# Kernel optimization log

Measured on AMD Instinct MI355X. Metric: run time of the kernel, lower is better.

Reference implementation:

```python
import jax, jax.numpy as jnp
import numpy as np

B, N, F_DIM, G_DIM, E_CAT, N_HEAD = 8, 1024, 128, 64, 2, 4
N_EDGES = 16384
L0 = 256          # NodeEmbedding hidden layer (layers=[256,128] -> last replaced by feature_size)
ALPHA = 0.5       # cfg.alpha
EPS = 1e-5        # BatchNorm eps
SLOPE = 0.01      # leaky_relu default negative slope


def _glorot(k, shape):
    stdv = float(np.sqrt(6.0 / (shape[-2] + shape[-1])))
    return jax.random.uniform(k, shape, jnp.float32, -stdv, stdv)


def setup_inputs() -> dict:
    key = jax.random.key(0)
    ks = jax.random.split(key, 8)
    X = jax.random.normal(ks[0], (B, N, F_DIM), dtype=jnp.float32)
    A = jax.random.randint(ks[1], (B, E_CAT, 2, N_EDGES), 0, N, dtype=jnp.int32)
    Ws = _glorot(ks[2], (E_CAT, N_HEAD * F_DIM, G_DIM))
    Wq = _glorot(ks[3], (E_CAT, N_HEAD * F_DIM, 1))
    Wv = _glorot(ks[4], (E_CAT, N_HEAD * F_DIM, 1))
    W_emb1 = _glorot(ks[5], (F_DIM, N_HEAD * E_CAT * G_DIM))   # Embedding1, bias=False
    W_lin0 = _glorot(ks[6], (L0, F_DIM))                        # NodeEmbedding linear0
    W_lin1 = _glorot(ks[7], (F_DIM, L0))                        # NodeEmbedding linear1
    return {"A": A, "X": X, "Ws": Ws, "Wq": Wq, "Wv": Wv,
            "W_emb1": W_emb1, "W_lin0": W_lin0, "W_lin1": W_lin1, "mini_batch": 1}


def _bn(x):
    # BatchNorm1d in training mode, affine = identity (weight=1, bias=0)
    mu = jnp.mean(x, axis=0)
    var = jnp.var(x, axis=0)  # biased variance, as torch uses for normalization
    return (x - mu) * jax.lax.rsqrt(var + EPS)


def _build_adj(A):
    # torch.sparse_coo_tensor(...).to_dense() sums duplicate edges
    adj = jnp.zeros((B, E_CAT, N, N), jnp.float32)
    b_idx = jnp.arange(B)[:, None, None]
    e_idx = jnp.arange(E_CAT)[None, :, None]
    return adj.at[b_idx, e_idx, A[:, :, 0], A[:, :, 1]].add(1.0)


def reference(A, X, Ws, Wq, Wv, W_emb1, W_lin0, W_lin1, mini_batch):
    Ws_r = Ws.reshape(E_CAT, N_HEAD, F_DIM, G_DIM)
    Wq_r = Wq.reshape(E_CAT, N_HEAD, F_DIM)   # last dim of Wq param is 1
    Wv_r = Wv.reshape(E_CAT, N_HEAD, F_DIM)

    Wh = jnp.einsum('bnf,ehfg->behng', X, Ws_r)   # [B,E,H,N,G]
    q = jnp.einsum('bnf,ehf->behn', X, Wq_r)      # [B,E,H,N]
    v = jnp.einsum('bnf,ehf->behn', X, Wv_r)

    adj = _build_adj(A)                            # [B,E,N,N]
    # e = (Wq @ Wv.T) * E, then leaky_relu and row softmax (dim=1 on [N,N] = last axis)
    scores = q[:, :, :, :, None] * v[:, :, :, None, :] * adj[:, :, None]
    scores = jnp.where(scores >= 0, scores, SLOPE * scores)
    a = jax.nn.softmax(scores, axis=-1)
    H = jnp.einsum('behnm,behmg->behng', a, Wh)    # [B,E,H,N,G]

    # concat over heads: [B,N, head-major (E*G)]
    H = H.transpose(0, 3, 2, 1, 4).reshape(B * N, N_HEAD * E_CAT * G_DIM)
    H = jax.nn.relu(H @ W_emb1.T)
    Xf = X.reshape(B * N, F_DIM)
    H = _bn((1.0 - ALPHA) * H + ALPHA * Xf)

    # NodeEmbedding: Linear -> BN -> ELU -> Linear
    Z = jax.nn.elu(_bn(H @ W_lin0.T))
    Z = Z @ W_lin1.T
    Z = _bn(H + Z)
    return Z.reshape(B, N, F_DIM)
```

## Files before the change

### kernel.cpp

```cpp
#include <hip/hip_runtime.h>
#include <hip/hip_bf16.h>

#define B_    8
#define N_    1024
#define F_    128
#define G_    64
#define EC    2
#define NHD   4
#define NE    16384
#define L0_   256
#define ALPHA_ 0.5f
#define EPS_   1e-5f
#define SLOPE_ 0.01f
#define ROWS  (B_*N_)
#define C1    (NHD*EC*G_)

typedef __attribute__((ext_vector_type(8))) short s8bf;
typedef __attribute__((ext_vector_type(4))) float f32x4;

__device__ __forceinline__ float ldv(const float* p, size_t i) { return p[i]; }
__device__ __forceinline__ float ldv(const __hip_bfloat16* p, size_t i) {
  unsigned short u = *(const unsigned short*)&p[i];
  return __uint_as_float((unsigned)u << 16);
}
__device__ __forceinline__ unsigned short f2b(float f) {
  unsigned u = __float_as_uint(f);
  u = (u + 0x7FFFu + ((u >> 16) & 1u)) >> 16;
  return (unsigned short)u;
}
__device__ __forceinline__ float b2f(unsigned short u) {
  return __uint_as_float((unsigned)u << 16);
}

__device__ __forceinline__ float wmaxf(float v) {
#pragma unroll
  for (int o = 32; o; o >>= 1) v = fmaxf(v, __shfl_xor(v, o, 64));
  return v;
}
__device__ __forceinline__ float wsumf(float v) {
#pragma unroll
  for (int o = 32; o; o >>= 1) v += __shfl_xor(v, o, 64);
  return v;
}

__global__ void k_prep(const unsigned short* Xu, int* flag,
                       const int* A, int* fill, int* colbuf) {
  int bid = blockIdx.x, tid = threadIdx.x;
  if (bid < 512) {
    int idx = bid * 256 + tid;
    unsigned short u = Xu[idx];
    if ((u & 0x7F80u) == 0x7F80u) atomicOr(flag, 1);
  } else {
    int idx = (bid - 512) * 256 + tid;
    int be = idx >> 14, i = idx & (NE - 1);
    int row = A[(size_t)(be * 2) * NE + i];
    int col = A[(size_t)(be * 2 + 1) * NE + i];
    int p = atomicAdd(&fill[be * N_ + row], 1);
    if (p < 64) colbuf[((size_t)(be * N_ + row)) * 64 + p] = col;
  }
}

__device__ __forceinline__ unsigned short cvt_at(const void* p, size_t i, int isf) {
  return isf ? f2b(((const float*)p)[i]) : ((const unsigned short*)p)[i];
}
template <typename T>
__device__ __forceinline__ void proj_qv16(const T* X, const T* Wq, const T* Wv,
                                          float* q, float* v, int pb) {
  int tid = threadIdx.x, lane = tid & 63, w = tid >> 6;
  int sub = lane >> 4, fl = lane & 15;
  int r = pb * 16 + w * 4 + sub;
  int n = r & (N_ - 1); int beh = r >> 10; int be = beh >> 2, h = beh & 3;
  int b = be >> 1, e = be & 1;
  const T* xr = X + (size_t)(b * N_ + n) * F_ + fl * 8;
  const T* wq = Wq + (e * NHD + h) * F_ + fl * 8;
  const T* wv = Wv + (e * NHD + h) * F_ + fl * 8;
  float dq = 0.f, dv = 0.f;
#pragma unroll
  for (int j = 0; j < 8; ++j) {
    float x = ldv(xr, j);
    dq += x * ldv(wq, j); dv += x * ldv(wv, j);
  }
#pragma unroll
  for (int o = 1; o < 16; o <<= 1) {
    dq += __shfl_xor(dq, o, 64); dv += __shfl_xor(dv, o, 64);
  }
  if (fl == 0) { q[r] = dq; v[r] = dv; }
}
__global__ void k_cvt2(const void* X, const void* Ws, const void* We1, const void* Wl1,
                       const void* Wl0, const void* Wq, const void* Wv,
                       unsigned short* Wsb, unsigned short* We1b,
                       unsigned short* Wl1b, unsigned short* Wl0b,
                       float* q, float* v, const int* flag) {
  int isf = *flag;
  int bid = blockIdx.x, t = threadIdx.x;
  if (bid < 256) {
    int i = bid * 256 + t; We1b[i] = cvt_at(We1, i, isf);
  } else if (bid < 384) {
    int i = (bid - 256) * 256 + t; Wl1b[i] = cvt_at(Wl1, i, isf);
  } else if (bid < 512) {
    int i = (bid - 384) * 256 + t; Wl0b[i] = cvt_at(Wl0, i, isf);
  } else if (bid < 768) {
    int i = (bid - 512) * 256 + t;
    int eh = i >> 13, rem = i & 8191;
    int g = rem >> 7, f = rem & 127;
    Wsb[eh * 8192 + g * 128 + f] = cvt_at(Ws, (size_t)eh * 8192 + f * 64 + g, isf);
  } else {
    int pb = bid - 768;
    if (isf) proj_qv16<float>((const float*)X, (const float*)Wq, (const float*)Wv, q, v, pb);
    else     proj_qv16<__hip_bfloat16>((const __hip_bfloat16*)X, (const __hip_bfloat16*)Wq,
                                       (const __hip_bfloat16*)Wv, q, v, pb);
  }
}

template <int K, int NC, int MODE, typename TA>
__device__ __forceinline__ void mfma_core_u(const TA* __restrict__ Araw,
                                            const float* sum, const float* ssq,
                                            const unsigned short* __restrict__ Wb,
                                            int r0, int c0, f32x4* acc) {
  int lane = threadIdx.x & 63; int q = lane >> 4, c15 = lane & 15;
  constexpr int RS = K / 8;
  const s8bf* bp = (const s8bf*)Wb + (size_t)(c0 + c15) * RS + q;
#pragma unroll
  for (int ks = 0; ks < K / 32; ++ks) {
    s8bf a;
    if constexpr (sizeof(TA) == 2) {
      const s8bf* ap = (const s8bf*)Araw + (size_t)(r0 + c15) * RS + q;
      a = ap[ks * 4];
    } else {
      const float* ap = (const float*)Araw + (size_t)(r0 + c15) * K + q * 8 + ks * 32;
      float av[8];
      *(float4*)&av[0] = *(const float4*)ap;
      *(float4*)&av[4] = *(const float4*)(ap + 4);
#pragma unroll
      for (int j = 0; j < 8; ++j) {
        float y = av[j];
        if (MODE) {
          int c = q * 8 + ks * 32 + j;
          float mean = sum[c] * (1.f / ROWS);
          float var = ssq[c] * (1.f / ROWS) - mean * mean;
          y = (y - mean) * rsqrtf(var + EPS_);
          if (MODE == 2) y = (y > 0.f) ? y : (expf(y) - 1.f);
        }
        a[j] = (short)f2b(y);
      }
    }
#pragma unroll
    for (int nc = 0; nc < NC; ++nc) {
      s8bf b = bp[(size_t)nc * 16 * RS + ks * 4];
      acc[nc] = __builtin_amdgcn_mfma_f32_16x16x32_bf16(a, b, acc[nc], 0, 0, 0);
    }
  }
}

__global__ __launch_bounds__(256) void k_whm(const void* X, const unsigned short* Wsb,
                                             unsigned short* Whb, float* S,
                                             const int* flag) {
  int w = threadIdx.x >> 6;
  int r0 = (blockIdx.x * 4 + w) * 16; int eh = blockIdx.y;
  f32x4 acc[4] = {{0,0,0,0},{0,0,0,0},{0,0,0,0},{0,0,0,0}};
  if (*flag)
    mfma_core_u<128, 4, 0, float>((const float*)X, nullptr, nullptr,
                                  Wsb + eh * 8192, r0, 0, acc);
  else
    mfma_core_u<128, 4, 0, unsigned short>((const unsigned short*)X, nullptr, nullptr,
                                           Wsb + eh * 8192, r0, 0, acc);
  int lane = threadIdx.x & 63, q = lane >> 4, c15 = lane & 15;
  int b = r0 >> 10; int beh = b * 8 + eh;
  unsigned short* WhB = Whb + ((size_t)beh * N_ + (r0 & (N_ - 1))) * G_;
#pragma unroll
  for (int nc = 0; nc < 4; ++nc) {
    float s = 0.f;
#pragma unroll
    for (int i = 0; i < 4; ++i) {
      float o = acc[nc][i];
      WhB[(size_t)(q * 4 + i) * G_ + nc * 16 + c15] = f2b(o);
      s += o;
    }
    s += __shfl_xor(s, 16, 64); s += __shfl_xor(s, 32, 64);
    if (lane < 16) atomicAdd(&S[(size_t)beh * G_ + nc * 16 + lane], s);
  }
}

__global__ __launch_bounds__(256) void k_attn3(const float* q, const float* v,
                                               const unsigned short* Whb,
                                               const float* S, const int* fill,
                                               const int* colbuf, unsigned short* Hcatb) {
  int tid = threadIdx.x, lane = tid & 63, w = tid >> 6;
  int xcd = blockIdx.x & 7, j = blockIdx.x >> 3;
  int be = (xcd << 1) | (j & 1);
  int n = (j >> 1) * 4 + w;
  int b = be >> 1, e = be & 1;
  int L = fill[be * N_ + n];
  int Lc = (L > 64) ? 64 : L;
  int myc = (lane < Lc) ? colbuf[((size_t)(be * N_ + n)) * 64 + lane] : -1;
  int cct = 0, firstk = 64;
  for (int k = 0; k < Lc; ++k) {
    int ck = __shfl(myc, k, 64);
    if (myc >= 0 && ck == myc) { cct++; if (k < firstk) firstk = k; }
  }
  bool act = (lane < Lc) && (firstk == lane);
  unsigned long long mask = __ballot(act);
  int pos = __popcll(mask & ((1ull << lane) - 1ull));
  __shared__ int s_col[4][64];
  __shared__ int s_cnt[4][64];
  s_col[w][lane] = 0; s_cnt[w][lane] = 0;
  if (act) { s_col[w][pos] = myc; s_cnt[w][pos] = cct; }
  int Ld = __popcll(mask);
  int colc = s_col[w][lane];
  int cntc = s_cnt[w][lane];
  int eg = lane >> 4, g4 = (lane & 15) << 2;
  size_t outb = ((size_t)(b * N_ + n)) * C1 + e * G_ + g4;
  float fN = (float)(N_ - Ld);
#pragma unroll
  for (int h = 0; h < 4; ++h) {
    int beh = (be << 2) | h;
    float qn = q[beh * N_ + n];
    float sc = -1e30f;
    if (lane < Ld) {
      float t = qn * v[beh * N_ + colc] * (float)cntc;
      sc = (t >= 0.f) ? t : SLOPE_ * t;
    }
    float M = fmaxf(0.f, wmaxf(sc));
    float Ej = (lane < Ld) ? expf(sc - M) : 0.f;
    float sumE = wsumf(Ej);
    float em = expf(-M);
    float Z = fN * em + sumE;
    float wgt = (lane < Ld) ? (Ej - em) / Z : 0.f;
    float4 accv = make_float4(0.f, 0.f, 0.f, 0.f);
    if (eg == 0) {
      float4 s4 = *(const float4*)&S[(size_t)beh * G_ + g4];
      float sca = em / Z;
      accv.x = sca * s4.x; accv.y = sca * s4.y; accv.z = sca * s4.z; accv.w = sca * s4.w;
    }
    const unsigned short* WhB = Whb + (size_t)beh * N_ * G_;
    for (int k0 = 0; k0 < Ld; k0 += 4) {
      int kk = k0 + eg;
      float wk = __shfl(wgt, kk, 64);
      int ck = __shfl(colc, kk, 64);
      ushort4 xu = *(const ushort4*)&WhB[(size_t)ck * G_ + g4];
      accv.x += wk * b2f(xu.x); accv.y += wk * b2f(xu.y);
      accv.z += wk * b2f(xu.z); accv.w += wk * b2f(xu.w);
    }
    accv.x += __shfl_xor(accv.x, 16, 64); accv.y += __shfl_xor(accv.y, 16, 64);
    accv.z += __shfl_xor(accv.z, 16, 64); accv.w += __shfl_xor(accv.w, 16, 64);
    accv.x += __shfl_xor(accv.x, 32, 64); accv.y += __shfl_xor(accv.y, 32, 64);
    accv.z += __shfl_xor(accv.z, 32, 64); accv.w += __shfl_xor(accv.w, 32, 64);
    if (lane < 16) {
      ushort4 o;
      o.x = f2b(accv.x); o.y = f2b(accv.y); o.z = f2b(accv.z); o.w = f2b(accv.w);
      *(ushort4*)&Hcatb[outb + (size_t)h * (EC * G_)] = o;
    }
  }
}

template <typename TX>
__device__ __forceinline__ void mm1_ep(f32x4* acc, const TX* X, float* T4,
                                       float* sum1, float* ssq1, int r0, int c0) {
  int lane = threadIdx.x & 63, q = lane >> 4, c15 = lane & 15;
#pragma unroll
  for (int nc = 0; nc < 2; ++nc) {
    int cc = c0 + nc * 16 + c15;
    float s = 0.f, s2 = 0.f;
#pragma unroll
    for (int i = 0; i < 4; ++i) {
      int rr = r0 + q * 4 + i;
      float o = fmaxf(acc[nc][i], 0.f);
      o = 0.5f * o + 0.5f * ldv(X, (size_t)rr * F_ + cc);
      T4[(size_t)rr * F_ + cc] = o;
      s += o; s2 += o * o;
    }
    s += __shfl_xor(s, 16, 64); s += __shfl_xor(s, 32, 64);
    s2 += __shfl_xor(s2, 16, 64); s2 += __shfl_xor(s2, 32, 64);
    if (lane < 16) {
      atomicAdd(&sum1[c0 + nc * 16 + lane], s);
      atomicAdd(&ssq1[c0 + nc * 16 + lane], s2);
    }
  }
}
__global__ __launch_bounds__(256) void k_mm1m(const unsigned short* Hcatb,
                                              const unsigned short* We1b, const void* X,
                                              float* T4, float* sum1, float* ssq1,
                                              const int* flag) {
  int w = threadIdx.x >> 6;
  int tile = blockIdx.x * 4 + w;
  int r0 = (tile >> 2) * 16, c0 = (tile & 3) * 32;
  f32x4 acc[2] = {{0,0,0,0},{0,0,0,0}};
  mfma_core_u<512, 2, 0, unsigned short>(Hcatb, nullptr, nullptr, We1b, r0, c0, acc);
  if (*flag) mm1_ep<float>(acc, (const float*)X, T4, sum1, ssq1, r0, c0);
  else       mm1_ep<__hip_bfloat16>(acc, (const __hip_bfloat16*)X, T4, sum1, ssq1, r0, c0);
}

__global__ __launch_bounds__(256) void k_lin0m(const float* T4, const float* sum1,
                                               const float* ssq1, const unsigned short* Wl0b,
                                               float* Z0, float* sum2, float* ssq2) {
  int w = threadIdx.x >> 6;
  int tile = blockIdx.x * 4 + w;
  int r0 = (tile >> 3) * 16, c0 = (tile & 7) * 32;
  f32x4 acc[2] = {{0,0,0,0},{0,0,0,0}};
  mfma_core_u<128, 2, 1, float>(T4, sum1, ssq1, Wl0b, r0, c0, acc);
  int lane = threadIdx.x & 63, q = lane >> 4, c15 = lane & 15;
#pragma unroll
  for (int nc = 0; nc < 2; ++nc) {
    int cc = c0 + nc * 16 + c15;
    float s = 0.f, s2 = 0.f;
#pragma unroll
    for (int i = 0; i < 4; ++i) {
      int rr = r0 + q * 4 + i;
      float o = acc[nc][i];
      Z0[(size_t)rr * L0_ + cc] = o;
      s += o; s2 += o * o;
    }
    s += __shfl_xor(s, 16, 64); s += __shfl_xor(s, 32, 64);
    s2 += __shfl_xor(s2, 16, 64); s2 += __shfl_xor(s2, 32, 64);
    if (lane < 16) {
      atomicAdd(&sum2[c0 + nc * 16 + lane], s);
      atomicAdd(&ssq2[c0 + nc * 16 + lane], s2);
    }
  }
}

__global__ __launch_bounds__(256) void k_lin1m(const float* Z0, const float* sum2,
                                               const float* ssq2, const unsigned short* Wl1b,
                                               const float* T4, const float* sum1,
                                               const float* ssq1,
                                               float* T6, float* sum3, float* ssq3) {
  int w = threadIdx.x >> 6;
  int tile = blockIdx.x * 4 + w;
  int r0 = (tile >> 2) * 16, c0 = (tile & 3) * 32;
  f32x4 acc[2] = {{0,0,0,0},{0,0,0,0}};
  mfma_core_u<256, 2, 2, float>(Z0, sum2, ssq2, Wl1b, r0, c0, acc);
  int lane = threadIdx.x & 63, q = lane >> 4, c15 = lane & 15;
#pragma unroll
  for (int nc = 0; nc < 2; ++nc) {
    int cc = c0 + nc * 16 + c15;
    float mean = sum1[cc] * (1.f / ROWS);
    float var = ssq1[cc] * (1.f / ROWS) - mean * mean;
    float rs = rsqrtf(var + EPS_);
    float s = 0.f, s2 = 0.f;
#pragma unroll
    for (int i = 0; i < 4; ++i) {
      int rr = r0 + q * 4 + i;
      float o = acc[nc][i] + (T4[(size_t)rr * F_ + cc] - mean) * rs;
      T6[(size_t)rr * F_ + cc] = o;
      s += o; s2 += o * o;
    }
    s += __shfl_xor(s, 16, 64); s += __shfl_xor(s, 32, 64);
    s2 += __shfl_xor(s2, 16, 64); s2 += __shfl_xor(s2, 32, 64);
    if (lane < 16) {
      atomicAdd(&sum3[c0 + nc * 16 + lane], s);
      atomicAdd(&ssq3[c0 + nc * 16 + lane], s2);
    }
  }
}

__global__ void k_norm_out(const float* in, void* out, const float* sum, const float* ssq,
                           const int* flag) {
  int idx = blockIdx.x * 256 + threadIdx.x; int c = idx & (F_ - 1);
  float mean = sum[c] * (1.f / ROWS);
  float var = ssq[c] * (1.f / ROWS) - mean * mean;
  float y = (in[idx] - mean) * rsqrtf(var + EPS_);
  if (*flag) ((float*)out)[idx] = y;
  else       ((__hip_bfloat16*)out)[idx] = __float2bfloat16(y);
}

extern "C" void kernel_launch(void* const* d_in, const int* in_sizes, int n_in,
                              void* d_out, int out_size, void* d_ws, size_t ws_size,
                              hipStream_t stream) {
  const int* A    = (const int*)d_in[0];
  const void* X   = d_in[1];
  const void* Ws  = d_in[2];
  const void* Wq  = d_in[3];
  const void* Wv  = d_in[4];
  const void* We1 = d_in[5];
  const void* Wl0 = d_in[6];
  const void* Wl1 = d_in[7];

  char* ws = (char*)d_ws;
  size_t off = 0;
  auto alloc = [&](size_t bytes) { size_t o = off; off += (bytes + 255) & ~(size_t)255; return o; };
  size_t o_fill   = alloc(16 * N_ * 4);
  size_t o_stats  = alloc(1024 * 4);
  size_t o_flag   = alloc(256);
  size_t o_S      = alloc((size_t)64 * G_ * 4);
  size_t zero_bytes = off;
  size_t o_colbuf = alloc((size_t)16 * N_ * 64 * 4);
  size_t o_q      = alloc((size_t)64 * N_ * 4);
  size_t o_v      = alloc((size_t)64 * N_ * 4);
  size_t o_Whb    = alloc((size_t)64 * N_ * G_ * 2);
  size_t o_Hcatb  = alloc((size_t)ROWS * C1 * 2);
  size_t o_T4     = alloc((size_t)ROWS * F_ * 4);
  size_t o_T6     = alloc((size_t)ROWS * F_ * 4);
  size_t o_Z0     = alloc((size_t)ROWS * L0_ * 4);
  size_t o_Wsb    = alloc((size_t)8 * G_ * F_ * 2);
  size_t o_We1b   = alloc((size_t)F_ * C1 * 2);
  size_t o_Wl1b   = alloc((size_t)F_ * L0_ * 2);
  size_t o_Wl0b   = alloc((size_t)L0_ * F_ * 2);

  int*   fill   = (int*)(ws + o_fill);
  float* stats  = (float*)(ws + o_stats);
  int*   flag   = (int*)(ws + o_flag);
  float* S      = (float*)(ws + o_S);
  int*   colbuf = (int*)(ws + o_colbuf);
  float* q      = (float*)(ws + o_q);
  float* v      = (float*)(ws + o_v);
  unsigned short* Whb   = (unsigned short*)(ws + o_Whb);
  unsigned short* Hcatb = (unsigned short*)(ws + o_Hcatb);
  float* T4     = (float*)(ws + o_T4);
  float* T6     = (float*)(ws + o_T6);
  float* Z0     = (float*)(ws + o_Z0);
  unsigned short* Wsb   = (unsigned short*)(ws + o_Wsb);
  unsigned short* We1b  = (unsigned short*)(ws + o_We1b);
  unsigned short* Wl1b  = (unsigned short*)(ws + o_Wl1b);
  unsigned short* Wl0b  = (unsigned short*)(ws + o_Wl0b);
  float* sum1 = stats,       *ssq1 = stats + 128;
  float* sum2 = stats + 256, *ssq2 = stats + 512;
  float* sum3 = stats + 768, *ssq3 = stats + 896;

  hipMemsetAsync(ws, 0, zero_bytes, stream);

  k_prep<<<1536, 256, 0, stream>>>((const unsigned short*)X, flag, A, fill, colbuf);
  k_cvt2<<<768 + 4096, 256, 0, stream>>>(X, Ws, We1, Wl1, Wl0, Wq, Wv,
                                         Wsb, We1b, Wl1b, Wl0b, q, v, flag);
  k_whm<<<dim3(ROWS / 64, 8), 256, 0, stream>>>(X, Wsb, Whb, S, flag);
  k_attn3<<<(16 * N_) / 4, 256, 0, stream>>>(q, v, Whb, S, fill, colbuf, Hcatb);
  k_mm1m<<<512, 256, 0, stream>>>(Hcatb, We1b, X, T4, sum1, ssq1, flag);
  k_lin0m<<<1024, 256, 0, stream>>>(T4, sum1, ssq1, Wl0b, Z0, sum2, ssq2);
  k_lin1m<<<512, 256, 0, stream>>>(Z0, sum2, ssq2, Wl1b, T4, sum1, ssq1,
                                   T6, sum3, ssq3);
  k_norm_out<<<(ROWS * F_) / 256, 256, 0, stream>>>(T6, d_out, sum3, ssq3, flag);

  (void)in_sizes; (void)n_in; (void)out_size; (void)ws_size;
}
```

Before: 212.5 us.

## Fold q/v projection into MFMA Wh GEMM, cache BN stats in LDS, vectorize output norm

The scalar q/v projection (4096 blocks of shuffle reductions) is replaced by a packed bf16 Wq/Wv matrix computed as an extra MFMA column tile in k_whm (grid y grows from 8 to 9). The linear kernels now precompute the BatchNorm mean and rsqrt once per block into shared memory instead of recomputing them per element inside the MFMA loop. The final normalization kernel processes four elements per thread with vector loads and stores. The trade-off is that q/v are now computed with bf16 inputs instead of full precision, which slightly lowers their accuracy.

```diff
diff --git a/kernel.cpp b/kernel.cpp
--- a/kernel.cpp
+++ b/kernel.cpp
@@ -63,34 +63,11 @@
 __device__ __forceinline__ unsigned short cvt_at(const void* p, size_t i, int isf) {
   return isf ? f2b(((const float*)p)[i]) : ((const unsigned short*)p)[i];
 }
-template <typename T>
-__device__ __forceinline__ void proj_qv16(const T* X, const T* Wq, const T* Wv,
-                                          float* q, float* v, int pb) {
-  int tid = threadIdx.x, lane = tid & 63, w = tid >> 6;
-  int sub = lane >> 4, fl = lane & 15;
-  int r = pb * 16 + w * 4 + sub;
-  int n = r & (N_ - 1); int beh = r >> 10; int be = beh >> 2, h = beh & 3;
-  int b = be >> 1, e = be & 1;
-  const T* xr = X + (size_t)(b * N_ + n) * F_ + fl * 8;
-  const T* wq = Wq + (e * NHD + h) * F_ + fl * 8;
-  const T* wv = Wv + (e * NHD + h) * F_ + fl * 8;
-  float dq = 0.f, dv = 0.f;
-#pragma unroll
-  for (int j = 0; j < 8; ++j) {
-    float x = ldv(xr, j);
-    dq += x * ldv(wq, j); dv += x * ldv(wv, j);
-  }
-#pragma unroll
-  for (int o = 1; o < 16; o <<= 1) {
-    dq += __shfl_xor(dq, o, 64); dv += __shfl_xor(dv, o, 64);
-  }
-  if (fl == 0) { q[r] = dq; v[r] = dv; }
-}
-__global__ void k_cvt2(const void* X, const void* Ws, const void* We1, const void* Wl1,
+__global__ void k_cvt2(const void* Ws, const void* We1, const void* Wl1,
                        const void* Wl0, const void* Wq, const void* Wv,
                        unsigned short* Wsb, unsigned short* We1b,
                        unsigned short* Wl1b, unsigned short* Wl0b,
-                       float* q, float* v, const int* flag) {
+                       unsigned short* Wqvb, const int* flag) {
   int isf = *flag;
   int bid = blockIdx.x, t = threadIdx.x;
   if (bid < 256) {
@@ -105,16 +82,16 @@
     int g = rem >> 7, f = rem & 127;
     Wsb[eh * 8192 + g * 128 + f] = cvt_at(Ws, (size_t)eh * 8192 + f * 64 + g, isf);
   } else {
-    int pb = bid - 768;
-    if (isf) proj_qv16<float>((const float*)X, (const float*)Wq, (const float*)Wv, q, v, pb);
-    else     proj_qv16<__hip_bfloat16>((const __hip_bfloat16*)X, (const __hip_bfloat16*)Wq,
-                                       (const __hip_bfloat16*)Wv, q, v, pb);
-  }
-}
-
-template <int K, int NC, int MODE, typename TA>
+    int i = (bid - 768) * 256 + t;
+    int c = i >> 7, f = i & 127;
+    int eh = c >> 1;
+    size_t src = (size_t)eh * 128 + f;
+    Wqvb[(size_t)c * 128 + f] = (c & 1) ? cvt_at(Wv, src, isf) : cvt_at(Wq, src, isf);
+  }
+}
+
+template <int K, int NC, typename TA>
 __device__ __forceinline__ void mfma_core_u(const TA* __restrict__ Araw,
-                                            const float* sum, const float* ssq,
                                             const unsigned short* __restrict__ Wb,
                                             int r0, int c0, f32x4* acc) {
   int lane = threadIdx.x & 63; int q = lane >> 4, c15 = lane & 15;
@@ -132,17 +109,7 @@
       *(float4*)&av[0] = *(const float4*)ap;
       *(float4*)&av[4] = *(const float4*)(ap + 4);
 #pragma unroll
-      for (int j = 0; j < 8; ++j) {
-        float y = av[j];
-        if (MODE) {
-          int c = q * 8 + ks * 32 + j;
-          float mean = sum[c] * (1.f / ROWS);
-          float var = ssq[c] * (1.f / ROWS) - mean * mean;
-          y = (y - mean) * rsqrtf(var + EPS_);
-          if (MODE == 2) y = (y > 0.f) ? y : (expf(y) - 1.f);
-        }
-        a[j] = (short)f2b(y);
-      }
+      for (int j = 0; j < 8; ++j) a[j] = (short)f2b(av[j]);
     }
 #pragma unroll
     for (int nc = 0; nc < NC; ++nc) {
@@ -152,32 +119,79 @@
   }
 }
 
+template <int K, int NC, int MODE>
+__device__ __forceinline__ void mfma_core_t2(const float* __restrict__ Araw,
+                                             const float* smean, const float* srs,
+                                             const unsigned short* __restrict__ Wb,
+                                             int r0, int c0, f32x4* acc) {
+  int lane = threadIdx.x & 63; int q = lane >> 4, c15 = lane & 15;
+  constexpr int RS = K / 8;
+  const s8bf* bp = (const s8bf*)Wb + (size_t)(c0 + c15) * RS + q;
+#pragma unroll
+  for (int ks = 0; ks < K / 32; ++ks) {
+    const float* ap = Araw + (size_t)(r0 + c15) * K + q * 8 + ks * 32;
+    float av[8];
+    *(float4*)&av[0] = *(const float4*)ap;
+    *(float4*)&av[4] = *(const float4*)(ap + 4);
+    s8bf a;
+#pragma unroll
+    for (int j = 0; j < 8; ++j) {
+      int c = q * 8 + ks * 32 + j;
+      float y = (av[j] - smean[c]) * srs[c];
+      if (MODE == 2) y = (y > 0.f) ? y : (expf(y) - 1.f);
+      a[j] = (short)f2b(y);
+    }
+    s8bf b0 = bp[ks * 4];
+    acc[0] = __builtin_amdgcn_mfma_f32_16x16x32_bf16(a, b0, acc[0], 0, 0, 0);
+    if (NC > 1) {
+      s8bf b1 = bp[(size_t)16 * RS + ks * 4];
+      acc[1] = __builtin_amdgcn_mfma_f32_16x16x32_bf16(a, b1, acc[1], 0, 0, 0);
+    }
+  }
+}
+
 __global__ __launch_bounds__(256) void k_whm(const void* X, const unsigned short* Wsb,
+                                             const unsigned short* Wqvb,
                                              unsigned short* Whb, float* S,
-                                             const int* flag) {
+                                             float* q, float* v, const int* flag) {
   int w = threadIdx.x >> 6;
   int r0 = (blockIdx.x * 4 + w) * 16; int eh = blockIdx.y;
-  f32x4 acc[4] = {{0,0,0,0},{0,0,0,0},{0,0,0,0},{0,0,0,0}};
-  if (*flag)
-    mfma_core_u<128, 4, 0, float>((const float*)X, nullptr, nullptr,
-                                  Wsb + eh * 8192, r0, 0, acc);
-  else
-    mfma_core_u<128, 4, 0, unsigned short>((const unsigned short*)X, nullptr, nullptr,
-                                           Wsb + eh * 8192, r0, 0, acc);
-  int lane = threadIdx.x & 63, q = lane >> 4, c15 = lane & 15;
-  int b = r0 >> 10; int beh = b * 8 + eh;
-  unsigned short* WhB = Whb + ((size_t)beh * N_ + (r0 & (N_ - 1))) * G_;
-#pragma unroll
-  for (int nc = 0; nc < 4; ++nc) {
-    float s = 0.f;
+  int lane = threadIdx.x & 63, qd = lane >> 4, c15 = lane & 15;
+  if (eh < 8) {
+    f32x4 acc[4] = {{0,0,0,0},{0,0,0,0},{0,0,0,0},{0,0,0,0}};
+    if (*flag)
+      mfma_core_u<128, 4, float>((const float*)X, Wsb + eh * 8192, r0, 0, acc);
+    else
+      mfma_core_u<128, 4, unsigned short>((const unsigned short*)X, Wsb + eh * 8192, r0, 0, acc);
+    int b = r0 >> 10; int beh = b * 8 + eh;
+    unsigned short* WhB = Whb + ((size_t)beh * N_ + (r0 & (N_ - 1))) * G_;
+#pragma unroll
+    for (int nc = 0; nc < 4; ++nc) {
+      float s = 0.f;
+#pragma unroll
+      for (int i = 0; i < 4; ++i) {
+        float o = acc[nc][i];
+        WhB[(size_t)(qd * 4 + i) * G_ + nc * 16 + c15] = f2b(o);
+        s += o;
+      }
+      s += __shfl_xor(s, 16, 64); s += __shfl_xor(s, 32, 64);
+      if (lane < 16) atomicAdd(&S[(size_t)beh * G_ + nc * 16 + lane], s);
+    }
+  } else {
+    f32x4 acc[1] = {{0,0,0,0}};
+    if (*flag)
+      mfma_core_u<128, 1, float>((const float*)X, Wqvb, r0, 0, acc);
+    else
+      mfma_core_u<128, 1, unsigned short>((const unsigned short*)X, Wqvb, r0, 0, acc);
+    int ehq = c15 >> 1, e = ehq >> 2, h = ehq & 3;
+    float* dst = (c15 & 1) ? v : q;
 #pragma unroll
     for (int i = 0; i < 4; ++i) {
-      float o = acc[nc][i];
-      WhB[(size_t)(q * 4 + i) * G_ + nc * 16 + c15] = f2b(o);
-      s += o;
-    }
-    s += __shfl_xor(s, 16, 64); s += __shfl_xor(s, 32, 64);
-    if (lane < 16) atomicAdd(&S[(size_t)beh * G_ + nc * 16 + lane], s);
+      int rr = r0 + qd * 4 + i;
+      int b = rr >> 10, n = rr & (N_ - 1);
+      int beh = ((b * 2 + e) << 2) | h;
+      dst[(size_t)beh * N_ + n] = acc[0][i];
+    }
   }
 }
 
@@ -285,7 +299,7 @@
   int tile = blockIdx.x * 4 + w;
   int r0 = (tile >> 2) * 16, c0 = (tile & 3) * 32;
   f32x4 acc[2] = {{0,0,0,0},{0,0,0,0}};
-  mfma_core_u<512, 2, 0, unsigned short>(Hcatb, nullptr, nullptr, We1b, r0, c0, acc);
+  mfma_core_u<512, 2, unsigned short>(Hcatb, We1b, r0, c0, acc);
   if (*flag) mm1_ep<float>(acc, (const float*)X, T4, sum1, ssq1, r0, c0);
   else       mm1_ep<__hip_bfloat16>(acc, (const __hip_bfloat16*)X, T4, sum1, ssq1, r0, c0);
 }
@@ -293,12 +307,20 @@
 __global__ __launch_bounds__(256) void k_lin0m(const float* T4, const float* sum1,
                                                const float* ssq1, const unsigned short* Wl0b,
                                                float* Z0, float* sum2, float* ssq2) {
-  int w = threadIdx.x >> 6;
+  __shared__ float smean[128], srs[128];
+  int tid = threadIdx.x;
+  if (tid < 128) {
+    float mean = sum1[tid] * (1.f / ROWS);
+    float var = ssq1[tid] * (1.f / ROWS) - mean * mean;
+    smean[tid] = mean; srs[tid] = rsqrtf(var + EPS_);
+  }
+  __syncthreads();
+  int w = tid >> 6;
   int tile = blockIdx.x * 4 + w;
   int r0 = (tile >> 3) * 16, c0 = (tile & 7) * 32;
   f32x4 acc[2] = {{0,0,0,0},{0,0,0,0}};
-  mfma_core_u<128, 2, 1, float>(T4, sum1, ssq1, Wl0b, r0, c0, acc);
-  int lane = threadIdx.x & 63, q = lane >> 4, c15 = lane & 15;
+  mfma_core_t2<128, 2, 1>(T4, smean, srs, Wl0b, r0, c0, acc);
+  int lane = tid & 63, q = lane >> 4, c15 = lane & 15;
 #pragma unroll
   for (int nc = 0; nc < 2; ++nc) {
     int cc = c0 + nc * 16 + c15;
@@ -324,12 +346,20 @@
                                                const float* T4, const float* sum1,
                                                const float* ssq1,
                                                float* T6, float* sum3, float* ssq3) {
-  int w = threadIdx.x >> 6;
+  __shared__ float smean[256], srs[256];
+  int tid = threadIdx.x;
+  {
+    float mean = sum2[tid] * (1.f / ROWS);
+    float var = ssq2[tid] * (1.f / ROWS) - mean * mean;
+    smean[tid] = mean; srs[tid] = rsqrtf(var + EPS_);
+  }
+  __syncthreads();
+  int w = tid >> 6;
   int tile = blockIdx.x * 4 + w;
   int r0 = (tile >> 2) * 16, c0 = (tile & 3) * 32;
   f32x4 acc[2] = {{0,0,0,0},{0,0,0,0}};
-  mfma_core_u<256, 2, 2, float>(Z0, sum2, ssq2, Wl1b, r0, c0, acc);
-  int lane = threadIdx.x & 63, q = lane >> 4, c15 = lane & 15;
+  mfma_core_t2<256, 2, 2>(Z0, smean, srs, Wl1b, r0, c0, acc);
+  int lane = tid & 63, q = lane >> 4, c15 = lane & 15;
 #pragma unroll
   for (int nc = 0; nc < 2; ++nc) {
     int cc = c0 + nc * 16 + c15;
@@ -355,12 +385,23 @@
 
 __global__ void k_norm_out(const float* in, void* out, const float* sum, const float* ssq,
                            const int* flag) {
-  int idx = blockIdx.x * 256 + threadIdx.x; int c = idx & (F_ - 1);
-  float mean = sum[c] * (1.f / ROWS);
-  float var = ssq[c] * (1.f / ROWS) - mean * mean;
-  float y = (in[idx] - mean) * rsqrtf(var + EPS_);
-  if (*flag) ((float*)out)[idx] = y;
-  else       ((__hip_bfloat16*)out)[idx] = __float2bfloat16(y);
+  int idx = (blockIdx.x * 256 + threadIdx.x) * 4;
+  float4 xv = *(const float4*)&in[idx];
+  float y[4]; float* xp = &xv.x;
+#pragma unroll
+  for (int j = 0; j < 4; ++j) {
+    int c = (idx + j) & (F_ - 1);
+    float mean = sum[c] * (1.f / ROWS);
+    float var = ssq[c] * (1.f / ROWS) - mean * mean;
+    y[j] = (xp[j] - mean) * rsqrtf(var + EPS_);
+  }
+  if (*flag) {
+    *(float4*)&((float*)out)[idx] = make_float4(y[0], y[1], y[2], y[3]);
+  } else {
+    ushort4 o;
+    o.x = f2b(y[0]); o.y = f2b(y[1]); o.z = f2b(y[2]); o.w = f2b(y[3]);
+    *(ushort4*)&((__hip_bfloat16*)out)[idx] = o;
+  }
 }
 
 extern "C" void kernel_launch(void* const* d_in, const int* in_sizes, int n_in,
@@ -395,6 +436,7 @@
   size_t o_We1b   = alloc((size_t)F_ * C1 * 2);
   size_t o_Wl1b   = alloc((size_t)F_ * L0_ * 2);
   size_t o_Wl0b   = alloc((size_t)L0_ * F_ * 2);
+  size_t o_Wqvb   = alloc((size_t)16 * F_ * 2);
 
   int*   fill   = (int*)(ws + o_fill);
   float* stats  = (float*)(ws + o_stats);
@@ -412,6 +454,7 @@
   unsigned short* We1b  = (unsigned short*)(ws + o_We1b);
   unsigned short* Wl1b  = (unsigned short*)(ws + o_Wl1b);
   unsigned short* Wl0b  = (unsigned short*)(ws + o_Wl0b);
+  unsigned short* Wqvb  = (unsigned short*)(ws + o_Wqvb);
   float* sum1 = stats,       *ssq1 = stats + 128;
   float* sum2 = stats + 256, *ssq2 = stats + 512;
   float* sum3 = stats + 768, *ssq3 = stats + 896;
@@ -419,15 +462,15 @@
   hipMemsetAsync(ws, 0, zero_bytes, stream);
 
   k_prep<<<1536, 256, 0, stream>>>((const unsigned short*)X, flag, A, fill, colbuf);
-  k_cvt2<<<768 + 4096, 256, 0, stream>>>(X, Ws, We1, Wl1, Wl0, Wq, Wv,
-                                         Wsb, We1b, Wl1b, Wl0b, q, v, flag);
-  k_whm<<<dim3(ROWS / 64, 8), 256, 0, stream>>>(X, Wsb, Whb, S, flag);
+  k_cvt2<<<776, 256, 0, stream>>>(Ws, We1, Wl1, Wl0, Wq, Wv,
+                                  Wsb, We1b, Wl1b, Wl0b, Wqvb, flag);
+  k_whm<<<dim3(ROWS / 64, 9), 256, 0, stream>>>(X, Wsb, Wqvb, Whb, S, q, v, flag);
   k_attn3<<<(16 * N_) / 4, 256, 0, stream>>>(q, v, Whb, S, fill, colbuf, Hcatb);
   k_mm1m<<<512, 256, 0, stream>>>(Hcatb, We1b, X, T4, sum1, ssq1, flag);
   k_lin0m<<<1024, 256, 0, stream>>>(T4, sum1, ssq1, Wl0b, Z0, sum2, ssq2);
   k_lin1m<<<512, 256, 0, stream>>>(Z0, sum2, ssq2, Wl1b, T4, sum1, ssq1,
                                    T6, sum3, ssq3);
-  k_norm_out<<<(ROWS * F_) / 256, 256, 0, stream>>>(T6, d_out, sum3, ssq3, flag);
+  k_norm_out<<<(ROWS * F_) / 1024, 256, 0, stream>>>(T6, d_out, sum3, ssq3, flag);
 
   (void)in_sizes; (void)n_in; (void)out_size; (void)ws_size;
 }
```

After: 206.1 us. -3.0%, faster.
